# Kernel optimization log

Measured on AMD Instinct MI355X. Metric: run time of the kernel, lower is better.

## Reference

```python
import jax, jax.numpy as jnp
import numpy as np

N = 1536; H = 32; L = 16; F = 8; B = 2
TRIU_I, TRIU_J = np.triu_indices(N, k=1)  # static pair indices, P = N(N-1)/2


def setup_inputs() -> dict:
    key = jax.random.key(0)
    ks = jax.random.split(key, 20)
    g = lambda k, shp, s=0.05: (jax.random.normal(k, shp) * s).astype(jnp.float32)
    inp = {
        'adj_matrix': jax.random.uniform(ks[0], (B, N, N), dtype=jnp.float32),
        'emb': g(ks[1], (N, F), 0.1),           # node_embedding table
        'W1': g(ks[2], (F, H)), 'b1': jnp.zeros((H,), jnp.float32),
        'W2': g(ks[3], (H, H)), 'b2': jnp.zeros((H,), jnp.float32),
        'W3': g(ks[4], (H, H)), 'b3': jnp.zeros((H,), jnp.float32),
        'Wmu': g(ks[5], (H, L)), 'bmu': jnp.zeros((L,), jnp.float32),
        'Wlv': g(ks[6], (H, L)), 'blv': jnp.zeros((L,), jnp.float32),
        'E1': g(ks[7], (2 * L, 2 * H)), 'e1': jnp.zeros((2 * H,), jnp.float32),
        'E2': g(ks[8], (2 * H, H)), 'e2': jnp.zeros((H,), jnp.float32),
        'E3': g(ks[9], (H, 1)), 'e3': jnp.zeros((1,), jnp.float32),
    }
    return inp


def reference(adj_matrix, emb, W1, b1, W2, b2, W3, b3, Wmu, bmu, Wlv, blv,
              E1, e1, E2, e2, E3, e3):
    A = adj_matrix  # [B, N, N], entries are edge weights (dense_to_sparse keeps nonzeros)
    diag = jnp.diagonal(A, axis1=1, axis2=2)                      # [B, N]
    # gcn_norm: add_remaining_self_loops -> self loop weight 1 only where missing
    fill = jnp.where(diag == 0.0, 1.0, diag)
    eye = jnp.eye(N, dtype=A.dtype)
    A_hat = A * (1.0 - eye) + eye * fill[:, :, None]              # [B, N, N]
    deg = A_hat.sum(-1)                                           # weighted degree
    dinv = jnp.where(deg > 0, deg ** -0.5, 0.0)[:, :, None]       # [B, N, 1]

    def prop(x):  # D^{-1/2} A_hat D^{-1/2} x
        return dinv * jnp.einsum('bij,bjf->bif', A_hat, dinv * x)

    x = jnp.broadcast_to(emb[None], (B, N, F))
    h1 = jax.nn.relu(prop(x @ W1) + b1)
    h2 = jax.nn.relu(prop(h1 @ W2) + b2) + h1
    h3 = jax.nn.relu(prop(h2 @ W3) + b3) + h2
    mu = h3 @ Wmu + bmu                                           # [B, N, L]
    logvar = h3 @ Wlv + blv
    z = mu  # eval-mode reparameterize

    # pairwise gather -> MLP -> symmetric scatter
    feats = jnp.concatenate([z[:, TRIU_I], z[:, TRIU_J]], axis=-1)  # [B, P, 2L]
    h = jax.nn.relu(feats @ E1 + e1)
    h = jax.nn.relu(h @ E2 + e2)
    w = jax.nn.sigmoid(h @ E3 + e3)[..., 0]                        # [B, P]
    adj_pred = jnp.zeros((B, N, N), z.dtype).at[:, TRIU_I, TRIU_J].set(w)
    adj_pred = adj_pred.at[:, TRIU_J, TRIU_I].set(w)
    return adj_pred, mu.reshape(B * N, L), logvar.reshape(B * N, L)
```

## Files before the change

kernel.cpp:

```cpp
#include <hip/hip_runtime.h>
#include <hip/hip_bf16.h>
#include <math.h>

#define Nn 1536
#define Bb 2
#define Hh 32
#define Ll 16
#define Nb 96
#define TREG 4656
#define KSTEPS 48

typedef short bf16x8 __attribute__((ext_vector_type(8)));
typedef _Float16 f16x8 __attribute__((ext_vector_type(8)));
typedef float f32x4 __attribute__((ext_vector_type(4)));
typedef short short4v __attribute__((ext_vector_type(4)));

__device__ __forceinline__ short f2bf(float x) {
    __hip_bfloat16 h = __float2bfloat16(x);
    return *reinterpret_cast<short*>(&h);
}

__device__ __forceinline__ float permswap32(float v) {
    float a = v, b = v;
    asm("v_permlane32_swap_b32 %0, %1" : "+v"(a), "+v"(b));
    return a;
}
__device__ __forceinline__ float permswap16(float v) {
    float a = v, b = v;
    asm("v_permlane16_swap_b32 %0, %1" : "+v"(a), "+v"(b));
    return a;
}

__global__ void prep_kernel(const float* __restrict__ A,
                            __hip_bfloat16* __restrict__ Abf,
                            float* __restrict__ dinv,
                            const float* __restrict__ emb,
                            const float* __restrict__ W1,
                            __hip_bfloat16* __restrict__ xsT) {
    int w = threadIdx.x >> 6;
    int lane = threadIdx.x & 63;
    int bi = blockIdx.x * 4 + w;
    if (bi >= Bb * Nn) return;
    int b = (bi >= Nn) ? 1 : 0;
    int i = bi - b * Nn;
    const float* Arow = A + (size_t)bi * Nn;
    short* Brow = (short*)Abf + (size_t)bi * Nn;
    float s = 0.f;
#pragma unroll
    for (int it = 0; it < 6; ++it) {
        int j = it * 256 + lane * 4;
        float4 a4 = *reinterpret_cast<const float4*>(Arow + j);
        s += a4.x + a4.y + a4.z + a4.w;
        float e0 = (j + 0 == i) ? ((a4.x == 0.f) ? 1.f : a4.x) : a4.x;
        float e1 = (j + 1 == i) ? ((a4.y == 0.f) ? 1.f : a4.y) : a4.y;
        float e2v = (j + 2 == i) ? ((a4.z == 0.f) ? 1.f : a4.z) : a4.z;
        float e3v = (j + 3 == i) ? ((a4.w == 0.f) ? 1.f : a4.w) : a4.w;
        short4v sv = { f2bf(e0), f2bf(e1), f2bf(e2v), f2bf(e3v) };
        *reinterpret_cast<short4v*>(Brow + j) = sv;
    }
#pragma unroll
    for (int o = 1; o < 64; o <<= 1) s += __shfl_xor(s, o, 64);
    float d = Arow[i];
    float fill = (d == 0.f) ? 1.f : d;
    float deg = s - d + fill;
    float di = (deg > 0.f) ? (1.f / sqrtf(deg)) : 0.f;
    if (lane == 0) dinv[bi] = di;
    if (lane < 32) {
        float acc = 0.f;
#pragma unroll
        for (int m = 0; m < 8; ++m)
            acc = fmaf(emb[(size_t)i * 8 + m], W1[m * Hh + lane], acc);
        ((short*)xsT)[(size_t)(b * Hh + lane) * Nn + i] = f2bf(di * acc);
    }
}

__global__ __launch_bounds__(256, 1) void prop_kernel(
    const __hip_bfloat16* __restrict__ Abf, const __hip_bfloat16* __restrict__ xsT,
    const float* __restrict__ dinv, const float* __restrict__ bias,
    const float* __restrict__ res, float* __restrict__ out, int has_res,
    const float* __restrict__ Wn, __hip_bfloat16* __restrict__ xsT_next,
    int final_stage,
    const float* __restrict__ Wmu, const float* __restrict__ bmu,
    const float* __restrict__ Wlv, const float* __restrict__ blv,
    const float* __restrict__ E1, const float* __restrict__ e1,
    float* __restrict__ mu, float* __restrict__ lv,
    _Float16* __restrict__ Uh, _Float16* __restrict__ Vh) {
    __shared__ float sRed[4][64][8];
    __shared__ float sOut[16][33];
    __shared__ float sWn[32][32];
    __shared__ float sMu[16][16];
    int t = threadIdx.x, lane = t & 63, w = t >> 6;
    int x = lane & 15, g = lane >> 4;
    int mt = blockIdx.x;
    int b = mt / Nb, it = mt - b * Nb;
    int i0 = it * 16;

    if (Wn) {
        for (int k = t; k < 1024; k += 256) sWn[k >> 5][k & 31] = Wn[k];
    }

    const short* Arow = (const short*)Abf + ((size_t)b * Nn + i0 + x) * Nn + 8 * g;
    const short* X0 = (const short*)xsT + ((size_t)(b * Hh) + x) * Nn + 8 * g;
    const short* X1 = X0 + (size_t)16 * Nn;

    f32x4 acc0 = {0.f, 0.f, 0.f, 0.f};
    f32x4 acc1 = {0.f, 0.f, 0.f, 0.f};
    int ks0 = w * (KSTEPS / 4);
#pragma unroll
    for (int ks = ks0; ks < ks0 + KSTEPS / 4; ++ks) {
        bf16x8 af = *reinterpret_cast<const bf16x8*>(Arow + ks * 32);
        bf16x8 b0 = *reinterpret_cast<const bf16x8*>(X0 + ks * 32);
        bf16x8 b1 = *reinterpret_cast<const bf16x8*>(X1 + ks * 32);
        acc0 = __builtin_amdgcn_mfma_f32_16x16x32_bf16(af, b0, acc0, 0, 0, 0);
        acc1 = __builtin_amdgcn_mfma_f32_16x16x32_bf16(af, b1, acc1, 0, 0, 0);
    }
#pragma unroll
    for (int r = 0; r < 4; ++r) { sRed[w][lane][r] = acc0[r]; sRed[w][lane][4 + r] = acc1[r]; }
    __syncthreads();

    int l = t & 63, xx = l & 15, gg = l >> 4;
#pragma unroll
    for (int q = 0; q < 2; ++q) {
        int ri = (t >> 6) * 2 + q;
        float v = sRed[0][l][ri] + sRed[1][l][ri] + sRed[2][l][ri] + sRed[3][l][ri];
        int row = 4 * gg + (ri & 3);
        int c = (ri < 4) ? xx : (16 + xx);
        int bi = b * Nn + i0 + row;
        v = dinv[bi] * v + bias[c];
        v = fmaxf(v, 0.f);
        if (has_res) v += res[(size_t)bi * Hh + c];
        out[(size_t)bi * Hh + c] = v;
        sOut[row][c] = v;
    }
    __syncthreads();

    if (Wn) {
        for (int k = t; k < 512; k += 256) {
            int r = k >> 5, c = k & 31;
            float acc = 0.f;
#pragma unroll
            for (int m = 0; m < 32; ++m) acc = fmaf(sOut[r][m], sWn[m][c], acc);
            int bi = b * Nn + i0 + r;
            ((short*)xsT_next)[(size_t)(b * Hh + c) * Nn + i0 + r] = f2bf(dinv[bi] * acc);
        }
    }
    if (final_stage) {
        {
            int r = t >> 4, ll = t & 15;
            float am = bmu[ll], av = blv[ll];
#pragma unroll
            for (int m = 0; m < 32; ++m) {
                float hv = sOut[r][m];
                am = fmaf(hv, Wmu[m * Ll + ll], am);
                av = fmaf(hv, Wlv[m * Ll + ll], av);
            }
            size_t o = ((size_t)b * Nn + i0 + r) * Ll + ll;
            mu[o] = am; lv[o] = av;
            sMu[r][ll] = am;
        }
        __syncthreads();
#pragma unroll
        for (int q = 0; q < 4; ++q) {
            int idx = q * 256 + t;
            int r = idx >> 6, c = idx & 63;
            float ua = e1[c], va = 0.f;
#pragma unroll
            for (int m = 0; m < Ll; ++m) {
                float zm = sMu[r][m];
                ua = fmaf(zm, E1[m * 64 + c], ua);
                va = fmaf(zm, E1[(16 + m) * 64 + c], va);
            }
            size_t o = ((size_t)b * Nn + i0 + r) * 64 + c;
            Uh[o] = (_Float16)ua;
            Vh[o] = (_Float16)va;
        }
    }
}

__global__ __launch_bounds__(256) void edge_kernel(
    const _Float16* __restrict__ Uh, const _Float16* __restrict__ Vh,
    const float* __restrict__ E2, const float* __restrict__ e2,
    const float* __restrict__ E3, const float* __restrict__ e3,
    float* __restrict__ adj) {
    __shared__ float sW[4][16][20];
    int t = threadIdx.x, lane = t & 63, w = t >> 6;
    int x = lane & 15, g = lane >> 4;

    f16x8 ea[2][2];
#pragma unroll
    for (int ct = 0; ct < 2; ++ct)
#pragma unroll
        for (int ks = 0; ks < 2; ++ks)
#pragma unroll
            for (int jj = 0; jj < 8; ++jj)
                ea[ct][ks][jj] = (_Float16)E2[(32 * ks + 8 * g + jj) * Hh + 16 * ct + x];

    float e2a[4], e2b[4], E3a[4], E3b[4];
#pragma unroll
    for (int rg = 0; rg < 4; ++rg) {
        e2a[rg] = e2[4 * g + rg];      E3a[rg] = E3[4 * g + rg];
        e2b[rg] = e2[16 + 4 * g + rg]; E3b[rg] = E3[16 + 4 * g + rg];
    }
    float e3s = e3[0];

    int tr = blockIdx.x * 4 + w;
    int b = 0;
    if (tr >= TREG) { b = 1; tr -= TREG; }
    float ft = (float)tr;
    int ib = (int)((193.0f - sqrtf(193.0f * 193.0f - 8.0f * ft)) * 0.5f);
    ib = ib < 0 ? 0 : (ib > Nb - 1 ? Nb - 1 : ib);
    while (ib < Nb - 1 && (ib + 1) * Nb - ((ib + 1) * ib) / 2 <= tr) ++ib;
    while (ib > 0 && ib * Nb - (ib * (ib - 1)) / 2 > tr) --ib;
    int jb = ib + (tr - (ib * Nb - (ib * (ib - 1)) / 2));
    int i0 = ib * 16, j0 = jb * 16;
    bool diag = (ib == jb);

    const f16x8* Vrow = reinterpret_cast<const f16x8*>(Vh + ((size_t)b * Nn + j0 + x) * 64);
    f16x8 vf0 = Vrow[g];
    f16x8 vf1 = Vrow[4 + g];

    const f16x8* Ubase = reinterpret_cast<const f16x8*>(Uh + ((size_t)b * Nn + i0) * 64);

    if (diag && lane < 16) sW[w][lane][lane] = 0.f;

    const f16x8 fz = {0, 0, 0, 0, 0, 0, 0, 0};
#pragma unroll 4
    for (int r = 0; r < 16; ++r) {
        f16x8 u0 = Ubase[r * 8 + g];
        f16x8 u1 = Ubase[r * 8 + 4 + g];

        f16x8 af0 = __builtin_elementwise_max(u0 + vf0, fz);
        f16x8 af1 = __builtin_elementwise_max(u1 + vf1, fz);

        f32x4 acc0 = {e2a[0], e2a[1], e2a[2], e2a[3]};
        f32x4 acc1 = {e2b[0], e2b[1], e2b[2], e2b[3]};
        acc0 = __builtin_amdgcn_mfma_f32_16x16x32_f16(ea[0][0], af0, acc0, 0, 0, 0);
        acc0 = __builtin_amdgcn_mfma_f32_16x16x32_f16(ea[0][1], af1, acc0, 0, 0, 0);
        acc1 = __builtin_amdgcn_mfma_f32_16x16x32_f16(ea[1][0], af0, acc1, 0, 0, 0);
        acc1 = __builtin_amdgcn_mfma_f32_16x16x32_f16(ea[1][1], af1, acc1, 0, 0, 0);

        float part = 0.f;
#pragma unroll
        for (int rg = 0; rg < 4; ++rg) {
            part = fmaf(fmaxf(acc0[rg], 0.f), E3a[rg], part);
            part = fmaf(fmaxf(acc1[rg], 0.f), E3b[rg], part);
        }
        part += permswap32(part);
        part += permswap16(part);

        float logit = part + e3s;
        float wv = __builtin_amdgcn_rcpf(1.f + __expf(-logit));

        if (g == 0) {
            if (!diag) {
                adj[((size_t)b * Nn + i0 + r) * Nn + j0 + x] = wv;
                sW[w][x][r] = wv;
            } else if (x > r) {
                sW[w][r][x] = wv;
                sW[w][x][r] = wv;
            }
        }
    }

    {
        int rr = lane >> 2, m4 = (lane & 3) * 4;
        float4 wv4 = *reinterpret_cast<const float4*>(&sW[w][rr][m4]);
        if (!diag)
            *reinterpret_cast<float4*>(&adj[((size_t)b * Nn + j0 + rr) * Nn + i0 + m4]) = wv4;
        else
            *reinterpret_cast<float4*>(&adj[((size_t)b * Nn + i0 + rr) * Nn + i0 + m4]) = wv4;
    }
}

extern "C" void kernel_launch(void* const* d_in, const int* in_sizes, int n_in,
                              void* d_out, int out_size, void* d_ws, size_t ws_size,
                              hipStream_t stream) {
    const float* A   = (const float*)d_in[0];
    const float* emb = (const float*)d_in[1];
    const float* W1  = (const float*)d_in[2];  const float* b1  = (const float*)d_in[3];
    const float* W2  = (const float*)d_in[4];  const float* b2  = (const float*)d_in[5];
    const float* W3  = (const float*)d_in[6];  const float* b3  = (const float*)d_in[7];
    const float* Wmu = (const float*)d_in[8];  const float* bmu = (const float*)d_in[9];
    const float* Wlv = (const float*)d_in[10]; const float* blv = (const float*)d_in[11];
    const float* E1  = (const float*)d_in[12]; const float* e1  = (const float*)d_in[13];
    const float* E2  = (const float*)d_in[14]; const float* e2  = (const float*)d_in[15];
    const float* E3  = (const float*)d_in[16]; const float* e3  = (const float*)d_in[17];

    float* out = (float*)d_out;
    float* ws  = (float*)d_ws;
    float* dinv = ws;
    float* hA   = ws + 3072;
    float* hB   = ws + 101376;
    __hip_bfloat16* xsTa = (__hip_bfloat16*)(ws + 199680);
    __hip_bfloat16* xsTb = (__hip_bfloat16*)(ws + 248832);
    _Float16* Uh = (_Float16*)(ws + 297984);
    _Float16* Vh = (_Float16*)(ws + 396288);
    __hip_bfloat16* Abf = (__hip_bfloat16*)out;

    float* mu_out = out + (size_t)Bb * Nn * Nn;
    float* lv_out = mu_out + (size_t)Bb * Nn * Ll;

    prep_kernel<<<(Bb * Nn + 3) / 4, 256, 0, stream>>>(A, Abf, dinv, emb, W1, xsTa);

    prop_kernel<<<Bb * Nb, 256, 0, stream>>>(Abf, xsTa, dinv, b1, nullptr, hA, 0,
                                             W2, xsTb, 0,
                                             nullptr, nullptr, nullptr, nullptr,
                                             nullptr, nullptr, nullptr, nullptr,
                                             nullptr, nullptr);
    prop_kernel<<<Bb * Nb, 256, 0, stream>>>(Abf, xsTb, dinv, b2, hA, hB, 1,
                                             W3, xsTa, 0,
                                             nullptr, nullptr, nullptr, nullptr,
                                             nullptr, nullptr, nullptr, nullptr,
                                             nullptr, nullptr);
    prop_kernel<<<Bb * Nb, 256, 0, stream>>>(Abf, xsTa, dinv, b3, hB, hA, 1,
                                             nullptr, nullptr, 1,
                                             Wmu, bmu, Wlv, blv, E1, e1,
                                             mu_out, lv_out, Uh, Vh);

    edge_kernel<<<(2 * TREG + 3) / 4, 256, 0, stream>>>(Uh, Vh, E2, e2, E3, e3, out);
}
```

Before: 68.67 us.

## Fuse prep and three GCN layers into one cooperative kernel with LDS-resident A

Measured after the change: 138.8 us. +102.1%, slower.

```diff
diff --git a/kernel.cpp b/kernel.cpp
--- a/kernel.cpp
+++ b/kernel.cpp
@@ -1,6 +1,9 @@
 #include <hip/hip_runtime.h>
+#include <hip/hip_cooperative_groups.h>
 #include <hip/hip_bf16.h>
 #include <math.h>
+
+namespace cg = cooperative_groups;
 
 #define Nn 1536
 #define Bb 2
@@ -31,149 +34,158 @@
     return a;
 }
 
-__global__ void prep_kernel(const float* __restrict__ A,
-                            __hip_bfloat16* __restrict__ Abf,
-                            float* __restrict__ dinv,
-                            const float* __restrict__ emb,
-                            const float* __restrict__ W1,
-                            __hip_bfloat16* __restrict__ xsT) {
-    int w = threadIdx.x >> 6;
-    int lane = threadIdx.x & 63;
-    int bi = blockIdx.x * 4 + w;
-    if (bi >= Bb * Nn) return;
-    int b = (bi >= Nn) ? 1 : 0;
-    int i = bi - b * Nn;
-    const float* Arow = A + (size_t)bi * Nn;
-    short* Brow = (short*)Abf + (size_t)bi * Nn;
-    float s = 0.f;
-#pragma unroll
-    for (int it = 0; it < 6; ++it) {
-        int j = it * 256 + lane * 4;
-        float4 a4 = *reinterpret_cast<const float4*>(Arow + j);
-        s += a4.x + a4.y + a4.z + a4.w;
-        float e0 = (j + 0 == i) ? ((a4.x == 0.f) ? 1.f : a4.x) : a4.x;
-        float e1 = (j + 1 == i) ? ((a4.y == 0.f) ? 1.f : a4.y) : a4.y;
-        float e2v = (j + 2 == i) ? ((a4.z == 0.f) ? 1.f : a4.z) : a4.z;
-        float e3v = (j + 3 == i) ? ((a4.w == 0.f) ? 1.f : a4.w) : a4.w;
-        short4v sv = { f2bf(e0), f2bf(e1), f2bf(e2v), f2bf(e3v) };
-        *reinterpret_cast<short4v*>(Brow + j) = sv;
-    }
-#pragma unroll
-    for (int o = 1; o < 64; o <<= 1) s += __shfl_xor(s, o, 64);
-    float d = Arow[i];
-    float fill = (d == 0.f) ? 1.f : d;
-    float deg = s - d + fill;
-    float di = (deg > 0.f) ? (1.f / sqrtf(deg)) : 0.f;
-    if (lane == 0) dinv[bi] = di;
-    if (lane < 32) {
-        float acc = 0.f;
-#pragma unroll
-        for (int m = 0; m < 8; ++m)
-            acc = fmaf(emb[(size_t)i * 8 + m], W1[m * Hh + lane], acc);
-        ((short*)xsT)[(size_t)(b * Hh + lane) * Nn + i] = f2bf(di * acc);
-    }
-}
-
-__global__ __launch_bounds__(256, 1) void prop_kernel(
-    const __hip_bfloat16* __restrict__ Abf, const __hip_bfloat16* __restrict__ xsT,
-    const float* __restrict__ dinv, const float* __restrict__ bias,
-    const float* __restrict__ res, float* __restrict__ out, int has_res,
-    const float* __restrict__ Wn, __hip_bfloat16* __restrict__ xsT_next,
-    int final_stage,
+__global__ __launch_bounds__(256, 1) void gcn_kernel(
+    const float* __restrict__ A, const float* __restrict__ emb,
+    const float* __restrict__ W1, const float* __restrict__ b1,
+    const float* __restrict__ W2, const float* __restrict__ b2,
+    const float* __restrict__ W3, const float* __restrict__ b3,
     const float* __restrict__ Wmu, const float* __restrict__ bmu,
     const float* __restrict__ Wlv, const float* __restrict__ blv,
     const float* __restrict__ E1, const float* __restrict__ e1,
+    __hip_bfloat16* __restrict__ xsTa, __hip_bfloat16* __restrict__ xsTb,
     float* __restrict__ mu, float* __restrict__ lv,
     _Float16* __restrict__ Uh, _Float16* __restrict__ Vh) {
+    __shared__ short sA[16][1544];
     __shared__ float sRed[4][64][8];
-    __shared__ float sOut[16][33];
-    __shared__ float sWn[32][32];
+    __shared__ float sH[16][33];
+    __shared__ float sWt[32][32];
     __shared__ float sMu[16][16];
+    __shared__ float sdinv[16];
+
+    cg::grid_group grid = cg::this_grid();
     int t = threadIdx.x, lane = t & 63, w = t >> 6;
     int x = lane & 15, g = lane >> 4;
     int mt = blockIdx.x;
     int b = mt / Nb, it = mt - b * Nb;
     int i0 = it * 16;
 
-    if (Wn) {
-        for (int k = t; k < 1024; k += 256) sWn[k >> 5][k & 31] = Wn[k];
-    }
-
-    const short* Arow = (const short*)Abf + ((size_t)b * Nn + i0 + x) * Nn + 8 * g;
-    const short* X0 = (const short*)xsT + ((size_t)(b * Hh) + x) * Nn + 8 * g;
-    const short* X1 = X0 + (size_t)16 * Nn;
-
-    f32x4 acc0 = {0.f, 0.f, 0.f, 0.f};
-    f32x4 acc1 = {0.f, 0.f, 0.f, 0.f};
-    int ks0 = w * (KSTEPS / 4);
-#pragma unroll
-    for (int ks = ks0; ks < ks0 + KSTEPS / 4; ++ks) {
-        bf16x8 af = *reinterpret_cast<const bf16x8*>(Arow + ks * 32);
-        bf16x8 b0 = *reinterpret_cast<const bf16x8*>(X0 + ks * 32);
-        bf16x8 b1 = *reinterpret_cast<const bf16x8*>(X1 + ks * 32);
-        acc0 = __builtin_amdgcn_mfma_f32_16x16x32_bf16(af, b0, acc0, 0, 0, 0);
-        acc1 = __builtin_amdgcn_mfma_f32_16x16x32_bf16(af, b1, acc1, 0, 0, 0);
-    }
-#pragma unroll
-    for (int r = 0; r < 4; ++r) { sRed[w][lane][r] = acc0[r]; sRed[w][lane][4 + r] = acc1[r]; }
+#pragma unroll 1
+    for (int rr = 0; rr < 4; ++rr) {
+        int r = w * 4 + rr;
+        int i = i0 + r;
+        const float* Arow = A + ((size_t)b * Nn + i) * Nn;
+        float s = 0.f;
+#pragma unroll
+        for (int itr = 0; itr < 6; ++itr) {
+            int j = itr * 256 + lane * 4;
+            float4 a4 = *reinterpret_cast<const float4*>(Arow + j);
+            s += a4.x + a4.y + a4.z + a4.w;
+            float v0 = (j + 0 == i) ? ((a4.x == 0.f) ? 1.f : a4.x) : a4.x;
+            float v1 = (j + 1 == i) ? ((a4.y == 0.f) ? 1.f : a4.y) : a4.y;
+            float v2 = (j + 2 == i) ? ((a4.z == 0.f) ? 1.f : a4.z) : a4.z;
+            float v3 = (j + 3 == i) ? ((a4.w == 0.f) ? 1.f : a4.w) : a4.w;
+            short4v sv = { f2bf(v0), f2bf(v1), f2bf(v2), f2bf(v3) };
+            *reinterpret_cast<short4v*>(&sA[r][j]) = sv;
+        }
+#pragma unroll
+        for (int o = 1; o < 64; o <<= 1) s += __shfl_xor(s, o, 64);
+        float d = Arow[i];
+        float fill = (d == 0.f) ? 1.f : d;
+        float deg = s - d + fill;
+        if (lane == 0) sdinv[r] = (deg > 0.f) ? (1.f / sqrtf(deg)) : 0.f;
+    }
     __syncthreads();
-
-    int l = t & 63, xx = l & 15, gg = l >> 4;
-#pragma unroll
-    for (int q = 0; q < 2; ++q) {
-        int ri = (t >> 6) * 2 + q;
-        float v = sRed[0][l][ri] + sRed[1][l][ri] + sRed[2][l][ri] + sRed[3][l][ri];
-        int row = 4 * gg + (ri & 3);
-        int c = (ri < 4) ? xx : (16 + xx);
-        int bi = b * Nn + i0 + row;
-        v = dinv[bi] * v + bias[c];
-        v = fmaxf(v, 0.f);
-        if (has_res) v += res[(size_t)bi * Hh + c];
-        out[(size_t)bi * Hh + c] = v;
-        sOut[row][c] = v;
+    {
+        int r = t & 15, c = (t >> 4) * 2;
+        int i = i0 + r;
+        float di = sdinv[r];
+        float acc0 = 0.f, acc1 = 0.f;
+#pragma unroll
+        for (int m = 0; m < 8; ++m) {
+            float ev = emb[(size_t)i * 8 + m];
+            acc0 = fmaf(ev, W1[m * Hh + c], acc0);
+            acc1 = fmaf(ev, W1[m * Hh + c + 1], acc1);
+        }
+        ((short*)xsTa)[(size_t)(b * Hh + c) * Nn + i] = f2bf(di * acc0);
+        ((short*)xsTa)[(size_t)(b * Hh + c + 1) * Nn + i] = f2bf(di * acc1);
+    }
+    grid.sync();
+
+    const __hip_bfloat16* xsCur = xsTa;
+    __hip_bfloat16* xsNext = xsTb;
+#pragma unroll 1
+    for (int layer = 0; layer < 3; ++layer) {
+        const float* bias = (layer == 0) ? b1 : (layer == 1) ? b2 : b3;
+        const float* Wnext = (layer == 0) ? W2 : (layer == 1) ? W3 : nullptr;
+        if (Wnext) {
+            for (int k = t; k < 1024; k += 256) sWt[k >> 5][k & 31] = Wnext[k];
+        }
+
+        const short* X0 = (const short*)xsCur + ((size_t)(b * Hh) + x) * Nn + 8 * g;
+        const short* X1 = X0 + (size_t)16 * Nn;
+        f32x4 acc0 = {0.f, 0.f, 0.f, 0.f};
+        f32x4 acc1 = {0.f, 0.f, 0.f, 0.f};
+        int ks0 = w * (KSTEPS / 4);
+#pragma unroll
+        for (int ks = ks0; ks < ks0 + KSTEPS / 4; ++ks) {
+            bf16x8 af = *reinterpret_cast<const bf16x8*>(&sA[x][ks * 32 + 8 * g]);
+            bf16x8 bb0 = *reinterpret_cast<const bf16x8*>(X0 + ks * 32);
+            bf16x8 bb1 = *reinterpret_cast<const bf16x8*>(X1 + ks * 32);
+            acc0 = __builtin_amdgcn_mfma_f32_16x16x32_bf16(af, bb0, acc0, 0, 0, 0);
+            acc1 = __builtin_amdgcn_mfma_f32_16x16x32_bf16(af, bb1, acc1, 0, 0, 0);
+        }
+#pragma unroll
+        for (int r = 0; r < 4; ++r) { sRed[w][lane][r] = acc0[r]; sRed[w][lane][4 + r] = acc1[r]; }
+        __syncthreads();
+        {
+            int xx = lane & 15, gg = lane >> 4;
+#pragma unroll
+            for (int q = 0; q < 2; ++q) {
+                int ri = w * 2 + q;
+                float v = sRed[0][lane][ri] + sRed[1][lane][ri] + sRed[2][lane][ri] + sRed[3][lane][ri];
+                int row = 4 * gg + (ri & 3);
+                int c = (ri < 4) ? xx : (16 + xx);
+                v = sdinv[row] * v + bias[c];
+                v = fmaxf(v, 0.f);
+                if (layer > 0) v += sH[row][c];
+                sH[row][c] = v;
+            }
+        }
+        __syncthreads();
+
+        if (Wnext) {
+            for (int k = t; k < 512; k += 256) {
+                int r = k & 15, c = k >> 4;
+                float acc = 0.f;
+#pragma unroll
+                for (int m = 0; m < 32; ++m) acc = fmaf(sH[r][m], sWt[m][c], acc);
+                ((short*)xsNext)[(size_t)(b * Hh + c) * Nn + i0 + r] = f2bf(sdinv[r] * acc);
+            }
+            const __hip_bfloat16* tmp = xsCur;
+            xsCur = xsNext;
+            xsNext = (__hip_bfloat16*)tmp;
+            grid.sync();
+        }
+    }
+
+    {
+        int r = t >> 4, ll = t & 15;
+        float am = bmu[ll], av = blv[ll];
+#pragma unroll
+        for (int m = 0; m < 32; ++m) {
+            float hv = sH[r][m];
+            am = fmaf(hv, Wmu[m * Ll + ll], am);
+            av = fmaf(hv, Wlv[m * Ll + ll], av);
+        }
+        size_t o = ((size_t)b * Nn + i0 + r) * Ll + ll;
+        mu[o] = am; lv[o] = av;
+        sMu[r][ll] = am;
     }
     __syncthreads();
-
-    if (Wn) {
-        for (int k = t; k < 512; k += 256) {
-            int r = k >> 5, c = k & 31;
-            float acc = 0.f;
-#pragma unroll
-            for (int m = 0; m < 32; ++m) acc = fmaf(sOut[r][m], sWn[m][c], acc);
-            int bi = b * Nn + i0 + r;
-            ((short*)xsT_next)[(size_t)(b * Hh + c) * Nn + i0 + r] = f2bf(dinv[bi] * acc);
-        }
-    }
-    if (final_stage) {
-        {
-            int r = t >> 4, ll = t & 15;
-            float am = bmu[ll], av = blv[ll];
-#pragma unroll
-            for (int m = 0; m < 32; ++m) {
-                float hv = sOut[r][m];
-                am = fmaf(hv, Wmu[m * Ll + ll], am);
-                av = fmaf(hv, Wlv[m * Ll + ll], av);
-            }
-            size_t o = ((size_t)b * Nn + i0 + r) * Ll + ll;
-            mu[o] = am; lv[o] = av;
-            sMu[r][ll] = am;
-        }
-        __syncthreads();
-#pragma unroll
-        for (int q = 0; q < 4; ++q) {
-            int idx = q * 256 + t;
-            int r = idx >> 6, c = idx & 63;
-            float ua = e1[c], va = 0.f;
-#pragma unroll
-            for (int m = 0; m < Ll; ++m) {
-                float zm = sMu[r][m];
-                ua = fmaf(zm, E1[m * 64 + c], ua);
-                va = fmaf(zm, E1[(16 + m) * 64 + c], va);
-            }
-            size_t o = ((size_t)b * Nn + i0 + r) * 64 + c;
-            Uh[o] = (_Float16)ua;
-            Vh[o] = (_Float16)va;
-        }
+#pragma unroll
+    for (int q = 0; q < 4; ++q) {
+        int idx = q * 256 + t;
+        int r = idx >> 6, c = idx & 63;
+        float ua = e1[c], va = 0.f;
+#pragma unroll
+        for (int m = 0; m < Ll; ++m) {
+            float zm = sMu[r][m];
+            ua = fmaf(zm, E1[m * 64 + c], ua);
+            va = fmaf(zm, E1[(16 + m) * 64 + c], va);
+        }
+        size_t o = ((size_t)b * Nn + i0 + r) * 64 + c;
+        Uh[o] = (_Float16)ua;
+        Vh[o] = (_Float16)va;
     }
 }
 
@@ -288,34 +300,24 @@
 
     float* out = (float*)d_out;
     float* ws  = (float*)d_ws;
-    float* dinv = ws;
-    float* hA   = ws + 3072;
-    float* hB   = ws + 101376;
-    __hip_bfloat16* xsTa = (__hip_bfloat16*)(ws + 199680);
-    __hip_bfloat16* xsTb = (__hip_bfloat16*)(ws + 248832);
-    _Float16* Uh = (_Float16*)(ws + 297984);
-    _Float16* Vh = (_Float16*)(ws + 396288);
-    __hip_bfloat16* Abf = (__hip_bfloat16*)out;
+    __hip_bfloat16* xsTa = (__hip_bfloat16*)(ws);
+    __hip_bfloat16* xsTb = (__hip_bfloat16*)(ws + 49152);
+    _Float16* Uh = (_Float16*)(ws + 98304);
+    _Float16* Vh = (_Float16*)(ws + 196608);
 
     float* mu_out = out + (size_t)Bb * Nn * Nn;
     float* lv_out = mu_out + (size_t)Bb * Nn * Ll;
 
-    prep_kernel<<<(Bb * Nn + 3) / 4, 256, 0, stream>>>(A, Abf, dinv, emb, W1, xsTa);
-
-    prop_kernel<<<Bb * Nb, 256, 0, stream>>>(Abf, xsTa, dinv, b1, nullptr, hA, 0,
-                                             W2, xsTb, 0,
-                                             nullptr, nullptr, nullptr, nullptr,
-                                             nullptr, nullptr, nullptr, nullptr,
-                                             nullptr, nullptr);
-    prop_kernel<<<Bb * Nb, 256, 0, stream>>>(Abf, xsTb, dinv, b2, hA, hB, 1,
-                                             W3, xsTa, 0,
-                                             nullptr, nullptr, nullptr, nullptr,
-                                             nullptr, nullptr, nullptr, nullptr,
-                                             nullptr, nullptr);
-    prop_kernel<<<Bb * Nb, 256, 0, stream>>>(Abf, xsTa, dinv, b3, hB, hA, 1,
-                                             nullptr, nullptr, 1,
-                                             Wmu, bmu, Wlv, blv, E1, e1,
-                                             mu_out, lv_out, Uh, Vh);
+    void* args[] = {
+        (void*)&A, (void*)&emb,
+        (void*)&W1, (void*)&b1, (void*)&W2, (void*)&b2, (void*)&W3, (void*)&b3,
+        (void*)&Wmu, (void*)&bmu, (void*)&Wlv, (void*)&blv,
+        (void*)&E1, (void*)&e1,
+        (void*)&xsTa, (void*)&xsTb,
+        (void*)&mu_out, (void*)&lv_out, (void*)&Uh, (void*)&Vh
+    };
+    hipLaunchCooperativeKernel((void*)gcn_kernel, dim3(Bb * Nb), dim3(256),
+                               args, 0, stream);
 
     edge_kernel<<<(2 * TREG + 3) / 4, 256, 0, stream>>>(Uh, Vh, E2, e2, E3, e3, out);
 }
```
